# Kernel optimization log

Hardware: AMD Instinct MI355X
Metric: run time of the kernel (lower is better)

## Reference

```python
import jax, jax.numpy as jnp
import numpy as np

N = 4_000_000   # number of sparse voxels
H = 128         # parent-grid extent per axis (input coords < 256 -> parents < 128)


def setup_inputs() -> dict:
    key = jax.random.key(0)
    # col 0 = batch index, cols 1:4 = integer xyz voxel coords in [0, 256)
    coords = jax.random.randint(key, (N, 4), 0, 256, dtype=jnp.int32)
    # spnn.Conv3d(1,1,k=2) kernel: (2^3, in=1, out=1), constant-init to 1.0
    kernel = jnp.ones((8, 1, 1), dtype=jnp.float32)
    return {"coords": coords, "kernel": kernel}


def _fog(coords, kernel):
    b = coords[:, 0].astype(jnp.int64)
    xyz = coords[:, 1:]
    # pos(): 3-bit occupancy code from LSBs of xyz, feat = 2^code
    bits = xyz & 1                                        # (N, 3)
    pos = bits[:, 0] + 2 * bits[:, 1] + 4 * bits[:, 2]    # (N,) in [0, 8)
    feats = (jnp.int32(1) << pos).astype(jnp.float32)     # (N,) values {1,...,128}

    # 2x2x2 stride-2 sparse conv with all-ones kernel == sum over the 8 children
    # of each parent voxel. The child's kernel-offset index is exactly `pos`.
    pxyz = (xyz >> 1).astype(jnp.int64)                   # parent coords
    pkey = ((b * H + pxyz[:, 0]) * H + pxyz[:, 1]) * H + pxyz[:, 2]

    ukeys, inv = jnp.unique(pkey, size=N, fill_value=-1, return_inverse=True)
    inv = inv.ravel()

    contrib = feats * kernel[pos, 0, 0]                   # all-ones kernel -> feats
    out_feats = jax.ops.segment_sum(contrib, inv, num_segments=N)  # (N,)

    # decode unique parent keys back to (batch, x, y, z); pad slots -> -1
    valid = ukeys >= 0
    k = jnp.where(valid, ukeys, 0)
    oz = k % H
    k = k // H
    oy = k % H
    k = k // H
    ox = k % H
    ob = k // H
    out_coords = jnp.stack([ob, ox, oy, oz], axis=-1).astype(jnp.int32)
    out_coords = jnp.where(valid[:, None], out_coords, jnp.int32(-1))
    return out_coords, out_feats


def reference(coords, kernel):
    return _fog(coords, kernel)
```

## Files before the change

### kernel.cpp

```cpp
#include <hip/hip_runtime.h>

#define NB_BITS     11
#define N_BUCKETS   (1 << NB_BITS)
#define LOCAL_BITS  18
#define LOCAL_WORDS 8192
#define LKMASK      ((1u << LOCAL_BITS) - 1u)
#define KEYMASK     0x1FFFFFFFu
#define NXCD        8
#define WCAP        512
#define WSHIFT      9
#define FE_CAP      2560
#define PPT         16
#define TILE        (1024 * PPT)

__device__ __forceinline__ unsigned make_key(int4 c) {
    return ((((unsigned)c.x << 7) | (unsigned)(c.y >> 1)) << 7 | (unsigned)(c.z >> 1)) << 7
         | (unsigned)(c.w >> 1);
}

template<int NW>
__device__ inline void block_scan(unsigned v, unsigned* wsum, unsigned& excl, unsigned& total) {
    int t = threadIdx.x, ln = t & 63, wv = t >> 6;
    unsigned incl = v;
    #pragma unroll
    for (int off = 1; off < 64; off <<= 1) {
        unsigned y = __shfl_up(incl, off, 64);
        if (ln >= off) incl += y;
    }
    if (ln == 63) wsum[wv] = incl;
    __syncthreads();
    if (wv == 0) {
        unsigned s = (ln < NW) ? wsum[ln] : 0u;
        #pragma unroll
        for (int off = 1; off < NW; off <<= 1) {
            unsigned y = __shfl_up(s, off, 64);
            if (ln >= off) s += y;
        }
        if (ln < NW) wsum[ln] = s;
    }
    __syncthreads();
    excl = (wv ? wsum[wv - 1] : 0u) + incl - v;
    total = wsum[NW - 1];
}

__global__ void __launch_bounds__(1024, 4)
build_pass(const int4* __restrict__ coords,
           unsigned* __restrict__ gcur,
           unsigned* __restrict__ pairs,
           int n) {
    __shared__ unsigned h[N_BUCKETS];
    int t = threadIdx.x, blk = blockIdx.x;
    unsigned xcd = (unsigned)blk & 7u;
    int base = blk * TILE;
    unsigned skey[PPT], lrank[PPT];
    h[t] = 0u; h[t + 1024] = 0u;
    #pragma unroll
    for (int m = 0; m < PPT; ++m) {
        int i = base + t + m * 1024;
        if (i < n) {
            int4 c = coords[i];
            unsigned key = make_key(c);
            unsigned pos = (unsigned)((c.y & 1) | ((c.z & 1) << 1) | ((c.w & 1) << 2));
            skey[m] = (pos << 29) | key;
        }
    }
    __syncthreads();
    #pragma unroll
    for (int m = 0; m < PPT; ++m) {
        int i = base + t + m * 1024;
        if (i < n)
            lrank[m] = atomicAdd(&h[(skey[m] & KEYMASK) >> LOCAL_BITS], 1u);
    }
    __syncthreads();
    #pragma unroll
    for (int q = 0; q < 2; ++q) {
        int j = t + q * 1024;
        unsigned c = h[j];
        if (c) h[j] = atomicAdd(&gcur[((unsigned)j << 3) | xcd], c);
    }
    __syncthreads();
    #pragma unroll
    for (int m = 0; m < PPT; ++m) {
        int i = base + t + m * 1024;
        if (i < n) {
            unsigned b = (skey[m] & KEYMASK) >> LOCAL_BITS;
            unsigned o = h[b] + lrank[m];
            if (o < WCAP)
                pairs[(((b << 3) | xcd) << WSHIFT) + o] = skey[m];
        }
    }
}

__global__ void __launch_bounds__(1024, 2)
count_pass(const unsigned* __restrict__ pairs,
           const unsigned* __restrict__ gcur,
           unsigned* __restrict__ ucount) {
    __shared__ unsigned bm[LOCAL_WORDS];
    __shared__ unsigned wsum[16];
    __shared__ unsigned gb[NXCD + 1];
    int t = threadIdx.x, b = blockIdx.x;
    ((uint4*)bm)[t] = make_uint4(0u, 0u, 0u, 0u);
    ((uint4*)bm)[t + 1024] = make_uint4(0u, 0u, 0u, 0u);
    if (t == 0) {
        unsigned r = 0;
        #pragma unroll
        for (int g = 0; g < NXCD; ++g) {
            gb[g] = r;
            r += min(gcur[((unsigned)b << 3) | g], (unsigned)WCAP);
        }
        gb[NXCD] = r;
    }
    __syncthreads();
    unsigned tot = gb[NXCD];
    for (unsigned p = (unsigned)t; p < tot; p += 1024) {
        unsigned g = 0;
        #pragma unroll
        for (int k = 1; k < NXCD; ++k) g += (p >= gb[k]) ? 1u : 0u;
        unsigned lk = pairs[((((unsigned)b << 3) | g) << WSHIFT) + (p - gb[g])] & LKMASK;
        atomicOr(&bm[lk >> 5], 1u << (lk & 31u));
    }
    __syncthreads();
    unsigned v = 0;
    #pragma unroll
    for (int m = 0; m < 8; ++m) v += __popc(bm[t + 1024 * m]);
    int ln = t & 63;
    #pragma unroll
    for (int off = 1; off < 64; off <<= 1) v += __shfl_xor(v, off, 64);
    if (ln == 0) wsum[t >> 6] = v;
    __syncthreads();
    if (t == 0) {
        unsigned c = 0;
        #pragma unroll
        for (int m = 0; m < 16; ++m) c += wsum[m];
        ucount[b] = c;
    }
}

__global__ void __launch_bounds__(1024, 2)
emit_pass(const unsigned* __restrict__ pairs,
          const unsigned* __restrict__ gcur,
          const unsigned* __restrict__ ucount,
          const float* __restrict__ kern,
          float4* __restrict__ out_coords,
          float* __restrict__ out_feats, int n) {
    __shared__ unsigned       bm[LOCAL_WORDS];
    __shared__ unsigned short pfx[LOCAL_WORDS];
    __shared__ float          fe[FE_CAP];
    __shared__ unsigned wsum[16];
    __shared__ unsigned gb[NXCD + 1];
    __shared__ unsigned ubS, totS;
    __shared__ float    kl[8];
    int t = threadIdx.x, b = blockIdx.x;
    if (t < 8) kl[t] = (float)(1 << t) * kern[t];
    ((uint4*)bm)[t] = make_uint4(0u, 0u, 0u, 0u);
    ((uint4*)bm)[t + 1024] = make_uint4(0u, 0u, 0u, 0u);
    for (int i = t; i < FE_CAP; i += 1024) fe[i] = 0.f;
    if (t == 0) {
        unsigned r = 0;
        #pragma unroll
        for (int g = 0; g < NXCD; ++g) {
            gb[g] = r;
            r += min(gcur[((unsigned)b << 3) | g], (unsigned)WCAP);
        }
        gb[NXCD] = r;
    }
    __syncthreads();
    unsigned tot = gb[NXCD];
    if (t < 64) {
        int ln = t;
        unsigned sum = 0;
        const uint4* uc4 = (const uint4*)ucount;
        #pragma unroll
        for (int q = 0; q < 8; ++q) {
            uint4 u = uc4[ln * 8 + q];
            sum += u.x + u.y + u.z + u.w;
        }
        unsigned incl = sum;
        #pragma unroll
        for (int off = 1; off < 64; off <<= 1) {
            unsigned y = __shfl_up(incl, off, 64);
            if (ln >= off) incl += y;
        }
        if (ln == 63) totS = incl;
        unsigned exclv = incl - sum;
        if (ln == (b >> 5)) {
            unsigned r = exclv;
            int lim = b & 31;
            for (int m = 0; m < lim; ++m) r += ucount[(b & ~31) + m];
            ubS = r;
        }
    } else {
        for (unsigned p = (unsigned)(t - 64); p < tot; p += 960) {
            unsigned g = 0;
            #pragma unroll
            for (int k = 1; k < NXCD; ++k) g += (p >= gb[k]) ? 1u : 0u;
            unsigned lk = pairs[((((unsigned)b << 3) | g) << WSHIFT) + (p - gb[g])] & LKMASK;
            atomicOr(&bm[lk >> 5], 1u << (lk & 31u));
        }
    }
    __syncthreads();
    uint4 q0 = ((uint4*)bm)[2 * t], q1 = ((uint4*)bm)[2 * t + 1];
    unsigned pc[8] = { (unsigned)__popc(q0.x), (unsigned)__popc(q0.y),
                       (unsigned)__popc(q0.z), (unsigned)__popc(q0.w),
                       (unsigned)__popc(q1.x), (unsigned)__popc(q1.y),
                       (unsigned)__popc(q1.z), (unsigned)__popc(q1.w) };
    unsigned psum = 0;
    #pragma unroll
    for (int m = 0; m < 8; ++m) psum += pc[m];
    unsigned excl, cnt;
    block_scan<16>(psum, wsum, excl, cnt);
    unsigned run = excl;
    #pragma unroll
    for (int m = 0; m < 8; ++m) { pfx[8 * t + m] = (unsigned short)run; run += pc[m]; }
    __syncthreads();
    unsigned ub = ubS;
    unsigned wq[8] = { q0.x, q0.y, q0.z, q0.w, q1.x, q1.y, q1.z, q1.w };
    unsigned r2 = excl;
    #pragma unroll
    for (int m = 0; m < 8; ++m) {
        unsigned w = wq[m];
        unsigned hi = ((unsigned)b << LOCAL_BITS) | ((unsigned)(8 * t + m) << 5);
        while (w) {
            unsigned bit = (unsigned)__ffs(w) - 1u;
            w &= w - 1u;
            unsigned key = hi | bit;
            out_coords[ub + r2] = make_float4((float)(key >> 21),
                                              (float)((key >> 14) & 127u),
                                              (float)((key >> 7) & 127u),
                                              (float)(key & 127u));
            ++r2;
        }
    }
    for (unsigned p = (unsigned)t; p < tot; p += 1024) {
        unsigned g = 0;
        #pragma unroll
        for (int k = 1; k < NXCD; ++k) g += (p >= gb[k]) ? 1u : 0u;
        unsigned pk = pairs[((((unsigned)b << 3) | g) << WSHIFT) + (p - gb[g])];
        unsigned lk = pk & LKMASK;
        unsigned wd = lk >> 5;
        unsigned lr = (unsigned)pfx[wd] + __popc(bm[wd] & ((1u << (lk & 31u)) - 1u));
        atomicAdd(&fe[lr], kl[pk >> 29]);
    }
    __syncthreads();
    for (unsigned i = (unsigned)t; i < cnt; i += 1024)
        out_feats[ub + i] = fe[i];
    for (unsigned r = totS + (unsigned)(b * 1024 + t); r < (unsigned)n; r += N_BUCKETS * 1024u) {
        out_coords[r] = make_float4(-1.f, -1.f, -1.f, -1.f);
        out_feats[r] = 0.f;
    }
}

extern "C" void kernel_launch(void* const* d_in, const int* in_sizes, int n_in,
                              void* d_out, int out_size, void* d_ws, size_t ws_size,
                              hipStream_t stream) {
    const int4* coords = (const int4*)d_in[0];
    const float* kern  = (const float*)d_in[1];
    int N = in_sizes[0] / 4;

    float* out = (float*)d_out;
    float4* out_coords = (float4*)out;
    float* out_feats = out + (size_t)4 * N;

    unsigned* pairs  = (unsigned*)d_ws;
    unsigned* gcur   = pairs + (size_t)N_BUCKETS * NXCD * WCAP;
    unsigned* ucount = gcur + (size_t)N_BUCKETS * NXCD;

    hipMemsetAsync(gcur, 0, (size_t)N_BUCKETS * NXCD * sizeof(unsigned), stream);

    int ntiles = (N + TILE - 1) / TILE;
    build_pass<<<ntiles, 1024, 0, stream>>>(coords, gcur, pairs, N);
    count_pass<<<N_BUCKETS, 1024, 0, stream>>>(pairs, gcur, ucount);
    emit_pass<<<N_BUCKETS, 1024, 0, stream>>>(pairs, gcur, ucount, kern, out_coords, out_feats, N);
}
```

Baseline: 208.9 us.

## Replace count pass with decoupled look-back prefix in emit pass

Removes the separate count_pass, which re-read all pairs to compute unique counts per bucket. emit_pass now publishes each bucket's unique count and resolves its global offset through a decoupled look-back over a status-flagged array, and a small tail_pass fills the padding. build_pass keeps keys in LDS instead of registers, halves the points per thread, and takes per-element ranks with a second atomic pass. The look-back assumes earlier blocks are scheduled first, which is a forward-progress risk, and the spin loop adds latency on the critical path.

```diff
diff --git a/kernel.cpp b/kernel.cpp
--- a/kernel.cpp
+++ b/kernel.cpp
@@ -10,8 +10,12 @@
 #define WCAP        512
 #define WSHIFT      9
 #define FE_CAP      2560
-#define PPT         16
+#define PPT         8
 #define TILE        (1024 * PPT)
+
+#define ST_AGG      (1u << 30)
+#define ST_PRE      (2u << 30)
+#define VALMASK     0x3FFFFFFFu
 
 __device__ __forceinline__ unsigned make_key(int4 c) {
     return ((((unsigned)c.x << 7) | (unsigned)(c.y >> 1)) << 7 | (unsigned)(c.z >> 1)) << 7
@@ -49,11 +53,12 @@
            unsigned* __restrict__ pairs,
            int n) {
     __shared__ unsigned h[N_BUCKETS];
+    __shared__ unsigned sk[TILE];
     int t = threadIdx.x, blk = blockIdx.x;
     unsigned xcd = (unsigned)blk & 7u;
     int base = blk * TILE;
-    unsigned skey[PPT], lrank[PPT];
     h[t] = 0u; h[t + 1024] = 0u;
+    __syncthreads();
     #pragma unroll
     for (int m = 0; m < PPT; ++m) {
         int i = base + t + m * 1024;
@@ -61,15 +66,10 @@
             int4 c = coords[i];
             unsigned key = make_key(c);
             unsigned pos = (unsigned)((c.y & 1) | ((c.z & 1) << 1) | ((c.w & 1) << 2));
-            skey[m] = (pos << 29) | key;
-        }
-    }
-    __syncthreads();
-    #pragma unroll
-    for (int m = 0; m < PPT; ++m) {
-        int i = base + t + m * 1024;
-        if (i < n)
-            lrank[m] = atomicAdd(&h[(skey[m] & KEYMASK) >> LOCAL_BITS], 1u);
+            unsigned s = (pos << 29) | key;
+            sk[t + m * 1024] = s;
+            atomicAdd(&h[key >> LOCAL_BITS], 1u);
+        }
     }
     __syncthreads();
     #pragma unroll
@@ -77,69 +77,26 @@
         int j = t + q * 1024;
         unsigned c = h[j];
         if (c) h[j] = atomicAdd(&gcur[((unsigned)j << 3) | xcd], c);
+        else   h[j] = 0u;
     }
     __syncthreads();
     #pragma unroll
     for (int m = 0; m < PPT; ++m) {
         int i = base + t + m * 1024;
         if (i < n) {
-            unsigned b = (skey[m] & KEYMASK) >> LOCAL_BITS;
-            unsigned o = h[b] + lrank[m];
+            unsigned s = sk[t + m * 1024];
+            unsigned b = (s & KEYMASK) >> LOCAL_BITS;
+            unsigned o = atomicAdd(&h[b], 1u);
             if (o < WCAP)
-                pairs[(((b << 3) | xcd) << WSHIFT) + o] = skey[m];
-        }
-    }
-}
-
-__global__ void __launch_bounds__(1024, 2)
-count_pass(const unsigned* __restrict__ pairs,
-           const unsigned* __restrict__ gcur,
-           unsigned* __restrict__ ucount) {
-    __shared__ unsigned bm[LOCAL_WORDS];
-    __shared__ unsigned wsum[16];
-    __shared__ unsigned gb[NXCD + 1];
-    int t = threadIdx.x, b = blockIdx.x;
-    ((uint4*)bm)[t] = make_uint4(0u, 0u, 0u, 0u);
-    ((uint4*)bm)[t + 1024] = make_uint4(0u, 0u, 0u, 0u);
-    if (t == 0) {
-        unsigned r = 0;
-        #pragma unroll
-        for (int g = 0; g < NXCD; ++g) {
-            gb[g] = r;
-            r += min(gcur[((unsigned)b << 3) | g], (unsigned)WCAP);
-        }
-        gb[NXCD] = r;
-    }
-    __syncthreads();
-    unsigned tot = gb[NXCD];
-    for (unsigned p = (unsigned)t; p < tot; p += 1024) {
-        unsigned g = 0;
-        #pragma unroll
-        for (int k = 1; k < NXCD; ++k) g += (p >= gb[k]) ? 1u : 0u;
-        unsigned lk = pairs[((((unsigned)b << 3) | g) << WSHIFT) + (p - gb[g])] & LKMASK;
-        atomicOr(&bm[lk >> 5], 1u << (lk & 31u));
-    }
-    __syncthreads();
-    unsigned v = 0;
-    #pragma unroll
-    for (int m = 0; m < 8; ++m) v += __popc(bm[t + 1024 * m]);
-    int ln = t & 63;
-    #pragma unroll
-    for (int off = 1; off < 64; off <<= 1) v += __shfl_xor(v, off, 64);
-    if (ln == 0) wsum[t >> 6] = v;
-    __syncthreads();
-    if (t == 0) {
-        unsigned c = 0;
-        #pragma unroll
-        for (int m = 0; m < 16; ++m) c += wsum[m];
-        ucount[b] = c;
+                pairs[(((b << 3) | xcd) << WSHIFT) + o] = s;
+        }
     }
 }
 
 __global__ void __launch_bounds__(1024, 2)
 emit_pass(const unsigned* __restrict__ pairs,
           const unsigned* __restrict__ gcur,
-          const unsigned* __restrict__ ucount,
+          unsigned* __restrict__ pub,
           const float* __restrict__ kern,
           float4* __restrict__ out_coords,
           float* __restrict__ out_feats, int n) {
@@ -148,7 +105,7 @@
     __shared__ float          fe[FE_CAP];
     __shared__ unsigned wsum[16];
     __shared__ unsigned gb[NXCD + 1];
-    __shared__ unsigned ubS, totS;
+    __shared__ unsigned ubS;
     __shared__ float    kl[8];
     int t = threadIdx.x, b = blockIdx.x;
     if (t < 8) kl[t] = (float)(1 << t) * kern[t];
@@ -166,37 +123,12 @@
     }
     __syncthreads();
     unsigned tot = gb[NXCD];
-    if (t < 64) {
-        int ln = t;
-        unsigned sum = 0;
-        const uint4* uc4 = (const uint4*)ucount;
-        #pragma unroll
-        for (int q = 0; q < 8; ++q) {
-            uint4 u = uc4[ln * 8 + q];
-            sum += u.x + u.y + u.z + u.w;
-        }
-        unsigned incl = sum;
-        #pragma unroll
-        for (int off = 1; off < 64; off <<= 1) {
-            unsigned y = __shfl_up(incl, off, 64);
-            if (ln >= off) incl += y;
-        }
-        if (ln == 63) totS = incl;
-        unsigned exclv = incl - sum;
-        if (ln == (b >> 5)) {
-            unsigned r = exclv;
-            int lim = b & 31;
-            for (int m = 0; m < lim; ++m) r += ucount[(b & ~31) + m];
-            ubS = r;
-        }
-    } else {
-        for (unsigned p = (unsigned)(t - 64); p < tot; p += 960) {
-            unsigned g = 0;
-            #pragma unroll
-            for (int k = 1; k < NXCD; ++k) g += (p >= gb[k]) ? 1u : 0u;
-            unsigned lk = pairs[((((unsigned)b << 3) | g) << WSHIFT) + (p - gb[g])] & LKMASK;
-            atomicOr(&bm[lk >> 5], 1u << (lk & 31u));
-        }
+    for (unsigned p = (unsigned)t; p < tot; p += 1024) {
+        unsigned g = 0;
+        #pragma unroll
+        for (int k = 1; k < NXCD; ++k) g += (p >= gb[k]) ? 1u : 0u;
+        unsigned lk = pairs[((((unsigned)b << 3) | g) << WSHIFT) + (p - gb[g])] & LKMASK;
+        atomicOr(&bm[lk >> 5], 1u << (lk & 31u));
     }
     __syncthreads();
     uint4 q0 = ((uint4*)bm)[2 * t], q1 = ((uint4*)bm)[2 * t + 1];
@@ -209,9 +141,46 @@
     for (int m = 0; m < 8; ++m) psum += pc[m];
     unsigned excl, cnt;
     block_scan<16>(psum, wsum, excl, cnt);
+    if (t == 0)
+        __hip_atomic_store(&pub[b], ST_AGG | cnt, __ATOMIC_RELAXED, __HIP_MEMORY_SCOPE_AGENT);
     unsigned run = excl;
     #pragma unroll
     for (int m = 0; m < 8; ++m) { pfx[8 * t + m] = (unsigned short)run; run += pc[m]; }
+    if (t < 64) {
+        unsigned sum = 0;
+        if (b > 0) {
+            int j = b - 1;
+            while (true) {
+                int idx = j - 63 + t;
+                unsigned v = (idx >= 0)
+                    ? __hip_atomic_load(&pub[idx], __ATOMIC_RELAXED, __HIP_MEMORY_SCOPE_AGENT)
+                    : (ST_PRE | 0u);
+                unsigned st = v >> 30;
+                unsigned long long vm = __ballot(st != 0u);
+                if (vm != ~0ull) continue;
+                unsigned long long pm = __ballot(st == 2u);
+                unsigned val = v & VALMASK;
+                if (pm) {
+                    int lp = 63 - __clzll(pm);
+                    unsigned red = (t >= lp) ? val : 0u;
+                    #pragma unroll
+                    for (int off = 1; off < 64; off <<= 1) red += __shfl_xor(red, off, 64);
+                    sum += red;
+                    break;
+                }
+                unsigned red = val;
+                #pragma unroll
+                for (int off = 1; off < 64; off <<= 1) red += __shfl_xor(red, off, 64);
+                sum += red;
+                j -= 64;
+            }
+        }
+        if (t == 0) {
+            __hip_atomic_store(&pub[b], ST_PRE | (sum + cnt),
+                               __ATOMIC_RELAXED, __HIP_MEMORY_SCOPE_AGENT);
+            ubS = sum;
+        }
+    }
     __syncthreads();
     unsigned ub = ubS;
     unsigned wq[8] = { q0.x, q0.y, q0.z, q0.w, q1.x, q1.y, q1.z, q1.w };
@@ -244,7 +213,15 @@
     __syncthreads();
     for (unsigned i = (unsigned)t; i < cnt; i += 1024)
         out_feats[ub + i] = fe[i];
-    for (unsigned r = totS + (unsigned)(b * 1024 + t); r < (unsigned)n; r += N_BUCKETS * 1024u) {
+}
+
+__global__ void tail_pass(const unsigned* __restrict__ pub,
+                          float4* __restrict__ out_coords,
+                          float* __restrict__ out_feats, int n) {
+    unsigned T = pub[N_BUCKETS - 1] & VALMASK;
+    unsigned gid = blockIdx.x * blockDim.x + threadIdx.x;
+    unsigned stride = gridDim.x * blockDim.x;
+    for (unsigned r = T + gid; r < (unsigned)n; r += stride) {
         out_coords[r] = make_float4(-1.f, -1.f, -1.f, -1.f);
         out_feats[r] = 0.f;
     }
@@ -261,14 +238,14 @@
     float4* out_coords = (float4*)out;
     float* out_feats = out + (size_t)4 * N;
 
-    unsigned* pairs  = (unsigned*)d_ws;
-    unsigned* gcur   = pairs + (size_t)N_BUCKETS * NXCD * WCAP;
-    unsigned* ucount = gcur + (size_t)N_BUCKETS * NXCD;
-
-    hipMemsetAsync(gcur, 0, (size_t)N_BUCKETS * NXCD * sizeof(unsigned), stream);
+    unsigned* pairs = (unsigned*)d_ws;
+    unsigned* gcur  = pairs + (size_t)N_BUCKETS * NXCD * WCAP;
+    unsigned* pub   = gcur + (size_t)N_BUCKETS * NXCD;
+
+    hipMemsetAsync(gcur, 0, (size_t)(N_BUCKETS * NXCD + N_BUCKETS) * sizeof(unsigned), stream);
 
     int ntiles = (N + TILE - 1) / TILE;
     build_pass<<<ntiles, 1024, 0, stream>>>(coords, gcur, pairs, N);
-    count_pass<<<N_BUCKETS, 1024, 0, stream>>>(pairs, gcur, ucount);
-    emit_pass<<<N_BUCKETS, 1024, 0, stream>>>(pairs, gcur, ucount, kern, out_coords, out_feats, N);
-}
+    emit_pass<<<N_BUCKETS, 1024, 0, stream>>>(pairs, gcur, pub, kern, out_coords, out_feats, N);
+    tail_pass<<<256, 256, 0, stream>>>(pub, out_coords, out_feats, N);
+}
```

Result: slower. 235.3 us (+12.6%).

## Add separate prefix-scan kernel, cache pair keys in registers, halve build tile

Applied to the files above, without the earlier changes.

A new single-block kernel scans the per-bucket unique counts once, replacing the per-block redundant scan of all counts that emit_pass used to do. Emit now loads each pair key once into registers and reuses it for the feature accumulation, so it no longer reads the pairs array a second time. The 8-entry bucket offsets are computed with a wave-level shuffle scan instead of a serial loop on thread 0. Build-pass items per thread are halved and emit's launch bounds raised to 8 blocks per SM. The cost is one extra kernel launch, and register caching assumes each bucket holds at most 4096 pairs.

```diff
diff --git a/kernel.cpp b/kernel.cpp
--- a/kernel.cpp
+++ b/kernel.cpp
@@ -10,7 +10,7 @@
 #define WCAP        512
 #define WSHIFT      9
 #define FE_CAP      2560
-#define PPT         16
+#define PPT         8
 #define TILE        (1024 * PPT)
 
 __device__ __forceinline__ unsigned make_key(int4 c) {
@@ -41,6 +41,22 @@
     __syncthreads();
     excl = (wv ? wsum[wv - 1] : 0u) + incl - v;
     total = wsum[NW - 1];
+}
+
+__device__ __forceinline__ void gb_setup(const unsigned* gcur, int b, unsigned* gb) {
+    int t = threadIdx.x;
+    unsigned gv = 0;
+    if (t < 8) gv = min(gcur[((unsigned)b << 3) | t], (unsigned)WCAP);
+    if (t < 64) {
+        unsigned incl = gv;
+        #pragma unroll
+        for (int off = 1; off < 8; off <<= 1) {
+            unsigned y = __shfl_up(incl, off, 64);
+            if (t >= off) incl += y;
+        }
+        if (t < 8) gb[t + 1] = incl;
+        if (t == 0) gb[0] = 0u;
+    }
 }
 
 __global__ void __launch_bounds__(1024, 4)
@@ -99,23 +115,15 @@
     __shared__ unsigned wsum[16];
     __shared__ unsigned gb[NXCD + 1];
     int t = threadIdx.x, b = blockIdx.x;
+    gb_setup(gcur, b, gb);
     ((uint4*)bm)[t] = make_uint4(0u, 0u, 0u, 0u);
     ((uint4*)bm)[t + 1024] = make_uint4(0u, 0u, 0u, 0u);
-    if (t == 0) {
-        unsigned r = 0;
-        #pragma unroll
-        for (int g = 0; g < NXCD; ++g) {
-            gb[g] = r;
-            r += min(gcur[((unsigned)b << 3) | g], (unsigned)WCAP);
-        }
-        gb[NXCD] = r;
-    }
     __syncthreads();
     unsigned tot = gb[NXCD];
-    for (unsigned p = (unsigned)t; p < tot; p += 1024) {
+    for (unsigned p = (unsigned)t; p < tot; p += 1024u) {
         unsigned g = 0;
         #pragma unroll
-        for (int k = 1; k < NXCD; ++k) g += (p >= gb[k]) ? 1u : 0u;
+        for (int j = 1; j < NXCD; ++j) g += (p >= gb[j]) ? 1u : 0u;
         unsigned lk = pairs[((((unsigned)b << 3) | g) << WSHIFT) + (p - gb[g])] & LKMASK;
         atomicOr(&bm[lk >> 5], 1u << (lk & 31u));
     }
@@ -136,10 +144,23 @@
     }
 }
 
-__global__ void __launch_bounds__(1024, 2)
+__global__ void __launch_bounds__(1024)
+prefix_pass(const unsigned* __restrict__ ucount,
+            unsigned* __restrict__ pbase) {
+    __shared__ unsigned wsum[16];
+    int t = threadIdx.x;
+    unsigned v0 = ucount[2 * t], v1 = ucount[2 * t + 1];
+    unsigned excl, total;
+    block_scan<16>(v0 + v1, wsum, excl, total);
+    pbase[2 * t] = excl;
+    pbase[2 * t + 1] = excl + v0;
+    if (t == 1023) pbase[N_BUCKETS] = total;
+}
+
+__global__ void __launch_bounds__(1024, 8)
 emit_pass(const unsigned* __restrict__ pairs,
           const unsigned* __restrict__ gcur,
-          const unsigned* __restrict__ ucount,
+          const unsigned* __restrict__ pbase,
           const float* __restrict__ kern,
           float4* __restrict__ out_coords,
           float* __restrict__ out_feats, int n) {
@@ -148,53 +169,27 @@
     __shared__ float          fe[FE_CAP];
     __shared__ unsigned wsum[16];
     __shared__ unsigned gb[NXCD + 1];
-    __shared__ unsigned ubS, totS;
     __shared__ float    kl[8];
     int t = threadIdx.x, b = blockIdx.x;
     if (t < 8) kl[t] = (float)(1 << t) * kern[t];
+    gb_setup(gcur, b, gb);
     ((uint4*)bm)[t] = make_uint4(0u, 0u, 0u, 0u);
     ((uint4*)bm)[t + 1024] = make_uint4(0u, 0u, 0u, 0u);
     for (int i = t; i < FE_CAP; i += 1024) fe[i] = 0.f;
-    if (t == 0) {
-        unsigned r = 0;
-        #pragma unroll
-        for (int g = 0; g < NXCD; ++g) {
-            gb[g] = r;
-            r += min(gcur[((unsigned)b << 3) | g], (unsigned)WCAP);
-        }
-        gb[NXCD] = r;
-    }
     __syncthreads();
     unsigned tot = gb[NXCD];
-    if (t < 64) {
-        int ln = t;
-        unsigned sum = 0;
-        const uint4* uc4 = (const uint4*)ucount;
-        #pragma unroll
-        for (int q = 0; q < 8; ++q) {
-            uint4 u = uc4[ln * 8 + q];
-            sum += u.x + u.y + u.z + u.w;
-        }
-        unsigned incl = sum;
-        #pragma unroll
-        for (int off = 1; off < 64; off <<= 1) {
-            unsigned y = __shfl_up(incl, off, 64);
-            if (ln >= off) incl += y;
-        }
-        if (ln == 63) totS = incl;
-        unsigned exclv = incl - sum;
-        if (ln == (b >> 5)) {
-            unsigned r = exclv;
-            int lim = b & 31;
-            for (int m = 0; m < lim; ++m) r += ucount[(b & ~31) + m];
-            ubS = r;
-        }
-    } else {
-        for (unsigned p = (unsigned)(t - 64); p < tot; p += 960) {
+    unsigned ub = pbase[b];
+    unsigned pk[4];
+    #pragma unroll
+    for (int k = 0; k < 4; ++k) {
+        unsigned p = (unsigned)t + (unsigned)k * 1024u;
+        if (p < tot) {
             unsigned g = 0;
             #pragma unroll
-            for (int k = 1; k < NXCD; ++k) g += (p >= gb[k]) ? 1u : 0u;
-            unsigned lk = pairs[((((unsigned)b << 3) | g) << WSHIFT) + (p - gb[g])] & LKMASK;
+            for (int j = 1; j < NXCD; ++j) g += (p >= gb[j]) ? 1u : 0u;
+            unsigned v = pairs[((((unsigned)b << 3) | g) << WSHIFT) + (p - gb[g])];
+            pk[k] = v;
+            unsigned lk = v & LKMASK;
             atomicOr(&bm[lk >> 5], 1u << (lk & 31u));
         }
     }
@@ -213,9 +208,8 @@
     #pragma unroll
     for (int m = 0; m < 8; ++m) { pfx[8 * t + m] = (unsigned short)run; run += pc[m]; }
     __syncthreads();
-    unsigned ub = ubS;
     unsigned wq[8] = { q0.x, q0.y, q0.z, q0.w, q1.x, q1.y, q1.z, q1.w };
-    unsigned r2 = excl;
+    unsigned rr = ub + excl;
     #pragma unroll
     for (int m = 0; m < 8; ++m) {
         unsigned w = wq[m];
@@ -224,27 +218,28 @@
             unsigned bit = (unsigned)__ffs(w) - 1u;
             w &= w - 1u;
             unsigned key = hi | bit;
-            out_coords[ub + r2] = make_float4((float)(key >> 21),
-                                              (float)((key >> 14) & 127u),
-                                              (float)((key >> 7) & 127u),
-                                              (float)(key & 127u));
-            ++r2;
-        }
-    }
-    for (unsigned p = (unsigned)t; p < tot; p += 1024) {
-        unsigned g = 0;
-        #pragma unroll
-        for (int k = 1; k < NXCD; ++k) g += (p >= gb[k]) ? 1u : 0u;
-        unsigned pk = pairs[((((unsigned)b << 3) | g) << WSHIFT) + (p - gb[g])];
-        unsigned lk = pk & LKMASK;
-        unsigned wd = lk >> 5;
-        unsigned lr = (unsigned)pfx[wd] + __popc(bm[wd] & ((1u << (lk & 31u)) - 1u));
-        atomicAdd(&fe[lr], kl[pk >> 29]);
-    }
-    __syncthreads();
-    for (unsigned i = (unsigned)t; i < cnt; i += 1024)
+            out_coords[rr++] = make_float4((float)(key >> 21),
+                                           (float)((key >> 14) & 127u),
+                                           (float)((key >> 7) & 127u),
+                                           (float)(key & 127u));
+        }
+    }
+    #pragma unroll
+    for (int k = 0; k < 4; ++k) {
+        unsigned p = (unsigned)t + (unsigned)k * 1024u;
+        if (p < tot) {
+            unsigned v = pk[k];
+            unsigned lk = v & LKMASK;
+            unsigned wd = lk >> 5;
+            unsigned lr = (unsigned)pfx[wd] + __popc(bm[wd] & ((1u << (lk & 31u)) - 1u));
+            atomicAdd(&fe[lr], kl[v >> 29]);
+        }
+    }
+    __syncthreads();
+    for (unsigned i = (unsigned)t; i < cnt; i += 1024u)
         out_feats[ub + i] = fe[i];
-    for (unsigned r = totS + (unsigned)(b * 1024 + t); r < (unsigned)n; r += N_BUCKETS * 1024u) {
+    unsigned T = pbase[N_BUCKETS];
+    for (unsigned r = T + (unsigned)(b * 1024 + t); r < (unsigned)n; r += N_BUCKETS * 1024u) {
         out_coords[r] = make_float4(-1.f, -1.f, -1.f, -1.f);
         out_feats[r] = 0.f;
     }
@@ -261,14 +256,17 @@
     float4* out_coords = (float4*)out;
     float* out_feats = out + (size_t)4 * N;
 
-    unsigned* pairs  = (unsigned*)d_ws;
-    unsigned* gcur   = pairs + (size_t)N_BUCKETS * NXCD * WCAP;
+    unsigned* gcur   = (unsigned*)d_ws;
     unsigned* ucount = gcur + (size_t)N_BUCKETS * NXCD;
+    unsigned* pbase  = ucount + (size_t)N_BUCKETS;
+    unsigned* pairs  = pbase + 2064;
 
     hipMemsetAsync(gcur, 0, (size_t)N_BUCKETS * NXCD * sizeof(unsigned), stream);
 
     int ntiles = (N + TILE - 1) / TILE;
     build_pass<<<ntiles, 1024, 0, stream>>>(coords, gcur, pairs, N);
     count_pass<<<N_BUCKETS, 1024, 0, stream>>>(pairs, gcur, ucount);
-    emit_pass<<<N_BUCKETS, 1024, 0, stream>>>(pairs, gcur, ucount, kern, out_coords, out_feats, N);
-}
+    prefix_pass<<<1, 1024, 0, stream>>>(ucount, pbase);
+    emit_pass<<<N_BUCKETS, 1024, 0, stream>>>(pairs, gcur, pbase, kern,
+                                              out_coords, out_feats, N);
+}
```

Result: slower. 217.4 us (+4.1%).
